# Performance work log

Measured on AMD Instinct MI355X. Metric: run time of the kernel, lower is better.

The kernel has to match this reference:

```python
import jax, jax.numpy as jnp
import numpy as np
import math

B, S, D, V = 16, 512, 64, 32000
MAX_SEQ = 512
TEMP = 1.0
EPS = 1e-12


def setup_inputs() -> dict:
    key = jax.random.key(0)
    k0, k1, k2, k3, k4 = jax.random.split(key, 5)
    tokens = jax.random.randint(k0, (B, S), 0, V)
    token_emb = jax.random.normal(k1, (V, D), dtype=jnp.float32) * 0.02
    lin_w1 = jax.random.normal(k2, (D, D), dtype=jnp.float32) * (1.0 / math.sqrt(D))
    lin_w2 = jax.random.normal(k3, (D, D), dtype=jnp.float32) * (1.0 / math.sqrt(D))
    edge_scale = jnp.full((1,), 0.1, dtype=jnp.float32)  # nn.Parameter init 0.1
    out_w = jax.random.normal(k4, (V, D), dtype=jnp.float32) * 0.02
    return {"tokens": tokens, "token_emb": token_emb, "lin_w1": lin_w1,
            "lin_w2": lin_w2, "edge_scale": edge_scale, "out_w": out_w}


def _embed(tokens, token_emb):
    # polar positional components (seq_len <= max_seq_len branch)
    pos = jnp.arange(S, dtype=jnp.float32)
    thetas = 2.0 * math.pi * (pos / MAX_SEQ)
    rs = 0.3 + 0.6 * (pos / (MAX_SEQ - 1))
    e0 = (rs * jnp.cos(thetas))[None, :, None]          # [1,S,1]
    e1 = (rs * jnp.sin(thetas))[None, :, None]          # [1,S,1]
    tok = token_emb[tokens][:, :, : D - 2]              # [B,S,D-2]
    emb = jnp.concatenate([jnp.broadcast_to(e0, (tok.shape[0], S, 1)),
                           jnp.broadcast_to(e1, (tok.shape[0], S, 1)),
                           tok], axis=-1)               # [B,S,D]
    norms = jnp.sqrt(jnp.clip(jnp.einsum('bsd,bsd->bs', emb, emb), EPS, None))
    return emb / norms[:, :, None]


def _attention(emb):
    # pairwise Euclidean distance attention, diagonal distance zeroed
    n2 = jnp.einsum('bsd,bsd->bs', emb, emb)                      # [B,S]
    dots = jnp.einsum('bqd,bkd->bqk', emb, emb)                   # [B,S,S]
    sq = n2[:, :, None] + n2[:, None, :] - 2.0 * dots
    dist = jnp.sqrt(jnp.clip(sq, EPS, None))
    dist = dist * (1.0 - jnp.eye(S, dtype=dist.dtype))[None]      # eye_mask
    return jax.nn.softmax(-dist / TEMP, axis=-1)                  # [B,S,S]


def reference(tokens, token_emb, lin_w1, lin_w2, edge_scale, out_w):
    emb = _embed(tokens, token_emb)            # [B,S,D]
    attn = _attention(emb)                     # [B,S,S]
    h = emb
    for w in (lin_w1, lin_w2):
        # message passing: x_j -> lin(x_j), edge weight = attn * edge_scale,
        # scatter-add over all incoming edges == batched attn @ h
        h = edge_scale[0] * jnp.einsum('bqk,bkd->bqd', attn, h @ w.T)
    logits = jnp.einsum('bsd,vd->bsv', h, out_w)   # [B,S,V]
    return logits
```

## Files before the change

kernel.cpp:

```cpp
#include <hip/hip_runtime.h>
#include <hip/hip_bf16.h>


#define S_ 512
#define D_ 64
#define V_ 32000

typedef __attribute__((ext_vector_type(8))) __bf16 bf16x8;
typedef __attribute__((ext_vector_type(4))) float f32x4;

__device__ inline unsigned short f2bf(float x) {
    __hip_bfloat16 h = __float2bfloat16(x);
    return __builtin_bit_cast(unsigned short, h);
}

__global__ __launch_bounds__(256) void embed_kernel(const int* __restrict__ tokens,
                                                    const float* __restrict__ temb,
                                                    float* __restrict__ emb,
                                                    float* __restrict__ n2) {
    int row  = blockIdx.x * 4 + (threadIdx.x >> 6);
    int lane = threadIdx.x & 63;
    int s    = row & (S_ - 1);
    int tok  = tokens[row];
    float val;
    if (lane < 2) {
        float fs    = (float)s;
        float theta = 6.283185307179586f * (fs * (1.0f / 512.0f));
        float r     = 0.3f + 0.6f * (fs * (1.0f / 511.0f));
        val = (lane == 0) ? r * cosf(theta) : r * sinf(theta);
    } else {
        val = temb[tok * D_ + lane - 2];
    }
    float ss = val * val;
#pragma unroll
    for (int off = 32; off; off >>= 1) ss += __shfl_xor(ss, off, 64);
    float nrm = sqrtf(fmaxf(ss, 1e-12f));
    float e   = val / nrm;
    emb[row * D_ + lane] = e;
    float nn = e * e;
#pragma unroll
    for (int off = 32; off; off >>= 1) nn += __shfl_xor(nn, off, 64);
    if (lane == 0) n2[row] = nn;
}

__global__ __launch_bounds__(128) void attn_kernel(const float* __restrict__ emb,
                                                   const float* __restrict__ n2,
                                                   float* __restrict__ attn) {
    __shared__ float qs[32][68];
    __shared__ float ks[64][68];
    __shared__ float sc[32][520];
    __shared__ float n2qs[32];
    __shared__ float n2ks[64];
    int b  = blockIdx.x >> 4;
    int q0 = (blockIdx.x & 15) * 32;
    int t  = threadIdx.x;
    const float* ebase = emb + (size_t)b * S_ * D_;
#pragma unroll
    for (int j = 0; j < 4; ++j) {
        int f4 = t + j * 128;
        int r = f4 >> 4, c4 = (f4 & 15) * 4;
        *reinterpret_cast<float4*>(&qs[r][c4]) =
            *reinterpret_cast<const float4*>(&ebase[(q0 + r) * D_ + c4]);
    }
    if (t < 32) n2qs[t] = n2[b * S_ + q0 + t];

    int qg = t >> 4;
    int kg = t & 15;

    for (int kt = 0; kt < 8; ++kt) {
        int k0 = kt * 64;
        __syncthreads();
#pragma unroll
        for (int j = 0; j < 8; ++j) {
            int f4 = t + j * 128;
            int r = f4 >> 4, c4 = (f4 & 15) * 4;
            *reinterpret_cast<float4*>(&ks[r][c4]) =
                *reinterpret_cast<const float4*>(&ebase[(k0 + r) * D_ + c4]);
        }
        if (t < 64) n2ks[t] = n2[b * S_ + k0 + t];
        __syncthreads();

        f32x4 acc[4][4];
#pragma unroll
        for (int i = 0; i < 4; ++i)
#pragma unroll
            for (int j = 0; j < 4; ++j) acc[i][j] = (f32x4){0.f, 0.f, 0.f, 0.f};
#pragma unroll
        for (int dc = 0; dc < 16; ++dc) {
            f32x4 qv[4], kv[4];
#pragma unroll
            for (int i = 0; i < 4; ++i) qv[i] = *reinterpret_cast<f32x4*>(&qs[qg * 4 + i][dc * 4]);
#pragma unroll
            for (int j = 0; j < 4; ++j) kv[j] = *reinterpret_cast<f32x4*>(&ks[kg * 4 + j][dc * 4]);
#pragma unroll
            for (int i = 0; i < 4; ++i)
#pragma unroll
                for (int j = 0; j < 4; ++j) acc[i][j] += qv[i] * kv[j];
        }
#pragma unroll
        for (int i = 0; i < 4; ++i)
#pragma unroll
            for (int j = 0; j < 4; ++j) {
                int q = qg * 4 + i, k = kg * 4 + j;
                f32x4 a = acc[i][j];
                float dot = (a[0] + a[1]) + (a[2] + a[3]);
                float sq  = n2qs[q] + n2ks[k] - 2.0f * dot;
                float sv  = (q0 + q == k0 + k) ? 0.0f : -sqrtf(fmaxf(sq, 1e-12f));
                sc[q][k0 + k] = sv;
            }
    }
    __syncthreads();
    int wave = t >> 6, lane = t & 63;
    for (int r = 0; r < 16; ++r) {
        int q = wave * 16 + r;
        f32x4 ex0, ex1;
        f32x4 v0 = *reinterpret_cast<f32x4*>(&sc[q][lane * 4]);
        f32x4 v1 = *reinterpret_cast<f32x4*>(&sc[q][256 + lane * 4]);
#pragma unroll
        for (int i = 0; i < 4; ++i) { ex0[i] = expf(v0[i]); ex1[i] = expf(v1[i]); }
        float sum = (ex0[0] + ex0[1]) + (ex0[2] + ex0[3]) +
                    (ex1[0] + ex1[1]) + (ex1[2] + ex1[3]);
#pragma unroll
        for (int off = 32; off; off >>= 1) sum += __shfl_xor(sum, off, 64);
        float inv = 1.0f / sum;
        float* row = attn + ((size_t)(b * S_ + q0 + q)) * S_;
        *reinterpret_cast<float4*>(row + lane * 4) =
            make_float4(ex0[0] * inv, ex0[1] * inv, ex0[2] * inv, ex0[3] * inv);
        *reinterpret_cast<float4*>(row + 256 + lane * 4) =
            make_float4(ex1[0] * inv, ex1[1] * inv, ex1[2] * inv, ex1[3] * inv);
    }
}

__global__ __launch_bounds__(256) void proj_kernel(const float* __restrict__ h,
                                                   const float* __restrict__ w,
                                                   float* __restrict__ out) {
    __shared__ float ws[64][68];
    __shared__ float hs[16][68];
    int t  = threadIdx.x;
    int r0 = blockIdx.x * 16;
#pragma unroll
    for (int j = 0; j < 4; ++j) {
        int f4 = t + j * 256;
        int r = f4 >> 4, c4 = (f4 & 15) * 4;
        *reinterpret_cast<float4*>(&ws[r][c4]) =
            *reinterpret_cast<const float4*>(&w[r * D_ + c4]);
    }
    {
        int r = t >> 4, c4 = (t & 15) * 4;
        *reinterpret_cast<float4*>(&hs[r][c4]) =
            *reinterpret_cast<const float4*>(&h[(r0 + r) * D_ + c4]);
    }
    __syncthreads();
    int q = t >> 4, dh = t & 15;
    f32x4 acc[4];
#pragma unroll
    for (int dj = 0; dj < 4; ++dj) acc[dj] = (f32x4){0.f, 0.f, 0.f, 0.f};
#pragma unroll
    for (int ec = 0; ec < 16; ++ec) {
        f32x4 hv = *reinterpret_cast<f32x4*>(&hs[q][ec * 4]);
#pragma unroll
        for (int dj = 0; dj < 4; ++dj) {
            f32x4 wv = *reinterpret_cast<f32x4*>(&ws[dh * 4 + dj][ec * 4]);
            acc[dj] += hv * wv;
        }
    }
    float4 r;
    r.x = (acc[0][0] + acc[0][1]) + (acc[0][2] + acc[0][3]);
    r.y = (acc[1][0] + acc[1][1]) + (acc[1][2] + acc[1][3]);
    r.z = (acc[2][0] + acc[2][1]) + (acc[2][2] + acc[2][3]);
    r.w = (acc[3][0] + acc[3][1]) + (acc[3][2] + acc[3][3]);
    *reinterpret_cast<float4*>(&out[(r0 + q) * D_ + dh * 4]) = r;
}

template <bool BF16OUT>
__global__ __launch_bounds__(128) void prop_kernel(const float* __restrict__ attn,
                                                   const float* __restrict__ tmat,
                                                   const float* __restrict__ edge_scale,
                                                   float* __restrict__ outf,
                                                   unsigned short* __restrict__ outb) {
    __shared__ float As[32][68];
    __shared__ float Ts[64][68];
    int b  = blockIdx.x >> 4;
    int q0 = (blockIdx.x & 15) * 32;
    int t  = threadIdx.x;
    int qg = t >> 4, dh = t & 15;
    f32x4 acc[4];
#pragma unroll
    for (int i = 0; i < 4; ++i) acc[i] = (f32x4){0.f, 0.f, 0.f, 0.f};
    const float* abase = attn + ((size_t)b * S_ + q0) * S_;
    const float* tbase = tmat + (size_t)b * S_ * D_;
    for (int kt = 0; kt < 8; ++kt) {
        int k0 = kt * 64;
        __syncthreads();
#pragma unroll
        for (int j = 0; j < 4; ++j) {
            int f4 = t + j * 128;
            int r = f4 >> 4, c4 = (f4 & 15) * 4;
            *reinterpret_cast<float4*>(&As[r][c4]) =
                *reinterpret_cast<const float4*>(&abase[(size_t)r * S_ + k0 + c4]);
        }
#pragma unroll
        for (int j = 0; j < 8; ++j) {
            int f4 = t + j * 128;
            int r = f4 >> 4, c4 = (f4 & 15) * 4;
            *reinterpret_cast<float4*>(&Ts[r][c4]) =
                *reinterpret_cast<const float4*>(&tbase[(k0 + r) * D_ + c4]);
        }
        __syncthreads();
#pragma unroll
        for (int kc = 0; kc < 16; ++kc) {
            f32x4 tv[4];
#pragma unroll
            for (int ks = 0; ks < 4; ++ks)
                tv[ks] = *reinterpret_cast<f32x4*>(&Ts[kc * 4 + ks][dh * 4]);
#pragma unroll
            for (int i = 0; i < 4; ++i) {
                f32x4 av = *reinterpret_cast<f32x4*>(&As[qg * 4 + i][kc * 4]);
#pragma unroll
                for (int ks = 0; ks < 4; ++ks) acc[i] += av[ks] * tv[ks];
            }
        }
    }
    float scale = edge_scale[0];
#pragma unroll
    for (int i = 0; i < 4; ++i) {
        size_t rowbase = ((size_t)(b * S_ + q0 + qg * 4 + i)) * D_ + dh * 4;
        if (BF16OUT) {
            ushort4 r;
            r.x = f2bf(scale * acc[i][0]); r.y = f2bf(scale * acc[i][1]);
            r.z = f2bf(scale * acc[i][2]); r.w = f2bf(scale * acc[i][3]);
            *reinterpret_cast<ushort4*>(&outb[rowbase]) = r;
        } else {
            *reinterpret_cast<float4*>(&outf[rowbase]) =
                make_float4(scale * acc[i][0], scale * acc[i][1],
                            scale * acc[i][2], scale * acc[i][3]);
        }
    }
}

__global__ __launch_bounds__(256) void cast_kernel(const float* __restrict__ in,
                                                   unsigned short* __restrict__ out, int n) {
    int i = (blockIdx.x * 256 + threadIdx.x) * 4;
    if (i >= n) return;
    float4 v = *reinterpret_cast<const float4*>(in + i);
    ushort4 r;
    r.x = f2bf(v.x); r.y = f2bf(v.y); r.z = f2bf(v.z); r.w = f2bf(v.w);
    *reinterpret_cast<ushort4*>(out + i) = r;
}

__global__ __launch_bounds__(256) void logits_kernel(const unsigned short* __restrict__ hb,
                                                     const unsigned short* __restrict__ wb,
                                                     float* __restrict__ out) {
    __shared__ float Ct[128][132];
    int bid = blockIdx.x;
    int nt = bid % 250, mt = bid / 250;
    int n0 = nt * 128, m0 = mt * 128;
    int wave = threadIdx.x >> 6, lane = threadIdx.x & 63;
    int nw = wave * 32;
    int lr = lane & 15, lh = lane >> 4;

    bf16x8 a[2][2];
#pragma unroll
    for (int ns = 0; ns < 2; ++ns)
#pragma unroll
        for (int kh = 0; kh < 2; ++kh)
            a[ns][kh] = *reinterpret_cast<const bf16x8*>(
                wb + (size_t)(n0 + nw + ns * 16 + lr) * D_ + kh * 32 + lh * 8);

    bf16x8 bfr[8][2];
#pragma unroll
    for (int ms = 0; ms < 8; ++ms)
#pragma unroll
        for (int kh = 0; kh < 2; ++kh)
            bfr[ms][kh] = *reinterpret_cast<const bf16x8*>(
                hb + (size_t)(m0 + ms * 16 + lr) * D_ + kh * 32 + lh * 8);

    f32x4 acc[2][8];
#pragma unroll
    for (int ns = 0; ns < 2; ++ns)
#pragma unroll
        for (int ms = 0; ms < 8; ++ms)
            acc[ns][ms] = (f32x4){0.f, 0.f, 0.f, 0.f};

#pragma unroll
    for (int ns = 0; ns < 2; ++ns)
#pragma unroll
        for (int ms = 0; ms < 8; ++ms) {
            acc[ns][ms] = __builtin_amdgcn_mfma_f32_16x16x32_bf16(a[ns][0], bfr[ms][0], acc[ns][ms], 0, 0, 0);
            acc[ns][ms] = __builtin_amdgcn_mfma_f32_16x16x32_bf16(a[ns][1], bfr[ms][1], acc[ns][ms], 0, 0, 0);
        }

#pragma unroll
    for (int ns = 0; ns < 2; ++ns)
#pragma unroll
        for (int ms = 0; ms < 8; ++ms) {
            f32x4 v = acc[ns][ms];
            *reinterpret_cast<float4*>(&Ct[ms * 16 + lr][nw + ns * 16 + lh * 4]) =
                make_float4(v[0], v[1], v[2], v[3]);
        }
    __syncthreads();

    int t = threadIdx.x;
    int r8 = t >> 5, c = (t & 31) * 4;
#pragma unroll
    for (int j = 0; j < 16; ++j) {
        int row = r8 + j * 8;
        *reinterpret_cast<float4*>(out + (size_t)(m0 + row) * V_ + n0 + c) =
            *reinterpret_cast<float4*>(&Ct[row][c]);
    }
}

extern "C" void kernel_launch(void* const* d_in, const int* in_sizes, int n_in,
                              void* d_out, int out_size, void* d_ws, size_t ws_size,
                              hipStream_t stream) {
    const int*   tokens = (const int*)d_in[0];
    const float* temb   = (const float*)d_in[1];
    const float* w1     = (const float*)d_in[2];
    const float* w2     = (const float*)d_in[3];
    const float* escale = (const float*)d_in[4];
    const float* outw   = (const float*)d_in[5];
    float*       out    = (float*)d_out;

    char* tail = (char*)d_out + 1048576000ull - 23068672ull;
    float* attn = (float*)(tail);
    float* emb  = (float*)(tail + 16777216);
    float* t1   = (float*)(tail + 18874368);
    float* h1   = (float*)(tail + 20971520);

    char* ws = (char*)d_ws;
    unsigned short* hb = (unsigned short*)(ws);
    unsigned short* wb = (unsigned short*)(ws + 1048576);
    float*          n2 = (float*)(ws + 5144576);

    embed_kernel<<<2048, 256, 0, stream>>>(tokens, temb, emb, n2);
    attn_kernel<<<256, 128, 0, stream>>>(emb, n2, attn);
    cast_kernel<<<2000, 256, 0, stream>>>(outw, wb, V_ * D_);
    proj_kernel<<<512, 256, 0, stream>>>(emb, w1, t1);
    prop_kernel<false><<<256, 128, 0, stream>>>(attn, t1, escale, h1, nullptr);
    proj_kernel<<<512, 256, 0, stream>>>(h1, w2, t1);
    prop_kernel<true><<<256, 128, 0, stream>>>(attn, t1, escale, nullptr, hb);
    logits_kernel<<<16000, 256, 0, stream>>>(hb, wb, out);
}
```

Before: 356.4 us.

## Defer softmax normalization into propagation and restructure logits kernel stores

```diff
diff --git a/kernel.cpp b/kernel.cpp
--- a/kernel.cpp
+++ b/kernel.cpp
@@ -45,10 +45,11 @@
 
 __global__ __launch_bounds__(128) void attn_kernel(const float* __restrict__ emb,
                                                    const float* __restrict__ n2,
-                                                   float* __restrict__ attn) {
+                                                   const float* __restrict__ edge_scale,
+                                                   float* __restrict__ attn_u,
+                                                   float* __restrict__ invs) {
     __shared__ float qs[32][68];
     __shared__ float ks[64][68];
-    __shared__ float sc[32][520];
     __shared__ float n2qs[32];
     __shared__ float n2ks[64];
     int b  = blockIdx.x >> 4;
@@ -66,6 +67,7 @@
 
     int qg = t >> 4;
     int kg = t & 15;
+    float rs[4] = {0.f, 0.f, 0.f, 0.f};
 
     for (int kt = 0; kt < 8; ++kt) {
         int k0 = kt * 64;
@@ -98,36 +100,30 @@
                 for (int j = 0; j < 4; ++j) acc[i][j] += qv[i] * kv[j];
         }
 #pragma unroll
-        for (int i = 0; i < 4; ++i)
+        for (int i = 0; i < 4; ++i) {
+            int q = qg * 4 + i;
+            float4 ev;
+            float* evp = &ev.x;
 #pragma unroll
             for (int j = 0; j < 4; ++j) {
-                int q = qg * 4 + i, k = kg * 4 + j;
+                int k = kg * 4 + j;
                 f32x4 a = acc[i][j];
                 float dot = (a[0] + a[1]) + (a[2] + a[3]);
                 float sq  = n2qs[q] + n2ks[k] - 2.0f * dot;
-                float sv  = (q0 + q == k0 + k) ? 0.0f : -sqrtf(fmaxf(sq, 1e-12f));
-                sc[q][k0 + k] = sv;
+                float e   = (q0 + q == k0 + k) ? 1.0f : expf(-sqrtf(fmaxf(sq, 1e-12f)));
+                evp[j] = e;
             }
-    }
-    __syncthreads();
-    int wave = t >> 6, lane = t & 63;
-    for (int r = 0; r < 16; ++r) {
-        int q = wave * 16 + r;
-        f32x4 ex0, ex1;
-        f32x4 v0 = *reinterpret_cast<f32x4*>(&sc[q][lane * 4]);
-        f32x4 v1 = *reinterpret_cast<f32x4*>(&sc[q][256 + lane * 4]);
-#pragma unroll
-        for (int i = 0; i < 4; ++i) { ex0[i] = expf(v0[i]); ex1[i] = expf(v1[i]); }
-        float sum = (ex0[0] + ex0[1]) + (ex0[2] + ex0[3]) +
-                    (ex1[0] + ex1[1]) + (ex1[2] + ex1[3]);
-#pragma unroll
-        for (int off = 32; off; off >>= 1) sum += __shfl_xor(sum, off, 64);
-        float inv = 1.0f / sum;
-        float* row = attn + ((size_t)(b * S_ + q0 + q)) * S_;
-        *reinterpret_cast<float4*>(row + lane * 4) =
-            make_float4(ex0[0] * inv, ex0[1] * inv, ex0[2] * inv, ex0[3] * inv);
-        *reinterpret_cast<float4*>(row + 256 + lane * 4) =
-            make_float4(ex1[0] * inv, ex1[1] * inv, ex1[2] * inv, ex1[3] * inv);
+            rs[i] += (ev.x + ev.y) + (ev.z + ev.w);
+            *reinterpret_cast<float4*>(
+                &attn_u[((size_t)(b * S_ + q0 + q)) * S_ + k0 + kg * 4]) = ev;
+        }
+    }
+    float scale = edge_scale[0];
+#pragma unroll
+    for (int i = 0; i < 4; ++i) {
+#pragma unroll
+        for (int off = 1; off < 16; off <<= 1) rs[i] += __shfl_xor(rs[i], off, 64);
+        if (kg == 0) invs[b * S_ + q0 + qg * 4 + i] = scale / rs[i];
     }
 }
 
@@ -173,9 +169,9 @@
 }
 
 template <bool BF16OUT>
-__global__ __launch_bounds__(128) void prop_kernel(const float* __restrict__ attn,
+__global__ __launch_bounds__(128) void prop_kernel(const float* __restrict__ attn_u,
                                                    const float* __restrict__ tmat,
-                                                   const float* __restrict__ edge_scale,
+                                                   const float* __restrict__ invs,
                                                    float* __restrict__ outf,
                                                    unsigned short* __restrict__ outb) {
     __shared__ float As[32][68];
@@ -187,7 +183,7 @@
     f32x4 acc[4];
 #pragma unroll
     for (int i = 0; i < 4; ++i) acc[i] = (f32x4){0.f, 0.f, 0.f, 0.f};
-    const float* abase = attn + ((size_t)b * S_ + q0) * S_;
+    const float* abase = attn_u + ((size_t)b * S_ + q0) * S_;
     const float* tbase = tmat + (size_t)b * S_ * D_;
     for (int kt = 0; kt < 8; ++kt) {
         int k0 = kt * 64;
@@ -221,19 +217,20 @@
             }
         }
     }
-    float scale = edge_scale[0];
 #pragma unroll
     for (int i = 0; i < 4; ++i) {
-        size_t rowbase = ((size_t)(b * S_ + q0 + qg * 4 + i)) * D_ + dh * 4;
+        int row = b * S_ + q0 + qg * 4 + i;
+        float inv = invs[row];
+        size_t rowbase = (size_t)row * D_ + dh * 4;
         if (BF16OUT) {
             ushort4 r;
-            r.x = f2bf(scale * acc[i][0]); r.y = f2bf(scale * acc[i][1]);
-            r.z = f2bf(scale * acc[i][2]); r.w = f2bf(scale * acc[i][3]);
+            r.x = f2bf(inv * acc[i][0]); r.y = f2bf(inv * acc[i][1]);
+            r.z = f2bf(inv * acc[i][2]); r.w = f2bf(inv * acc[i][3]);
             *reinterpret_cast<ushort4*>(&outb[rowbase]) = r;
         } else {
             *reinterpret_cast<float4*>(&outf[rowbase]) =
-                make_float4(scale * acc[i][0], scale * acc[i][1],
-                            scale * acc[i][2], scale * acc[i][3]);
+                make_float4(inv * acc[i][0], inv * acc[i][1],
+                            inv * acc[i][2], inv * acc[i][3]);
         }
     }
 }
@@ -251,12 +248,12 @@
 __global__ __launch_bounds__(256) void logits_kernel(const unsigned short* __restrict__ hb,
                                                      const unsigned short* __restrict__ wb,
                                                      float* __restrict__ out) {
-    __shared__ float Ct[128][132];
-    int bid = blockIdx.x;
-    int nt = bid % 250, mt = bid / 250;
-    int n0 = nt * 128, m0 = mt * 128;
+    int orig = blockIdx.x;
+    int wg   = (orig & 7) * 1000 + (orig >> 3);
+    int nt = wg % 250, mt = wg / 250;
+    int n0 = nt * 128, m0 = mt * 256;
     int wave = threadIdx.x >> 6, lane = threadIdx.x & 63;
-    int nw = wave * 32;
+    int nw = n0 + wave * 32;
     int lr = lane & 15, lh = lane >> 4;
 
     bf16x8 a[2][2];
@@ -265,48 +262,22 @@
 #pragma unroll
         for (int kh = 0; kh < 2; ++kh)
             a[ns][kh] = *reinterpret_cast<const bf16x8*>(
-                wb + (size_t)(n0 + nw + ns * 16 + lr) * D_ + kh * 32 + lh * 8);
-
-    bf16x8 bfr[8][2];
-#pragma unroll
-    for (int ms = 0; ms < 8; ++ms)
-#pragma unroll
-        for (int kh = 0; kh < 2; ++kh)
-            bfr[ms][kh] = *reinterpret_cast<const bf16x8*>(
-                hb + (size_t)(m0 + ms * 16 + lr) * D_ + kh * 32 + lh * 8);
-
-    f32x4 acc[2][8];
-#pragma unroll
-    for (int ns = 0; ns < 2; ++ns)
-#pragma unroll
-        for (int ms = 0; ms < 8; ++ms)
-            acc[ns][ms] = (f32x4){0.f, 0.f, 0.f, 0.f};
-
-#pragma unroll
-    for (int ns = 0; ns < 2; ++ns)
-#pragma unroll
-        for (int ms = 0; ms < 8; ++ms) {
-            acc[ns][ms] = __builtin_amdgcn_mfma_f32_16x16x32_bf16(a[ns][0], bfr[ms][0], acc[ns][ms], 0, 0, 0);
-            acc[ns][ms] = __builtin_amdgcn_mfma_f32_16x16x32_bf16(a[ns][1], bfr[ms][1], acc[ns][ms], 0, 0, 0);
-        }
-
-#pragma unroll
-    for (int ns = 0; ns < 2; ++ns)
-#pragma unroll
-        for (int ms = 0; ms < 8; ++ms) {
-            f32x4 v = acc[ns][ms];
-            *reinterpret_cast<float4*>(&Ct[ms * 16 + lr][nw + ns * 16 + lh * 4]) =
-                make_float4(v[0], v[1], v[2], v[3]);
-        }
-    __syncthreads();
-
-    int t = threadIdx.x;
-    int r8 = t >> 5, c = (t & 31) * 4;
-#pragma unroll
-    for (int j = 0; j < 16; ++j) {
-        int row = r8 + j * 8;
-        *reinterpret_cast<float4*>(out + (size_t)(m0 + row) * V_ + n0 + c) =
-            *reinterpret_cast<float4*>(&Ct[row][c]);
+                wb + (size_t)(nw + ns * 16 + lr) * D_ + kh * 32 + lh * 8);
+
+#pragma unroll 4
+    for (int ms = 0; ms < 16; ++ms) {
+        const unsigned short* hrow = hb + (size_t)(m0 + ms * 16 + lr) * D_ + lh * 8;
+        bf16x8 b0 = *reinterpret_cast<const bf16x8*>(hrow);
+        bf16x8 b1 = *reinterpret_cast<const bf16x8*>(hrow + 32);
+        f32x4 acc0 = (f32x4){0.f, 0.f, 0.f, 0.f};
+        f32x4 acc1 = (f32x4){0.f, 0.f, 0.f, 0.f};
+        acc0 = __builtin_amdgcn_mfma_f32_16x16x32_bf16(a[0][0], b0, acc0, 0, 0, 0);
+        acc0 = __builtin_amdgcn_mfma_f32_16x16x32_bf16(a[0][1], b1, acc0, 0, 0, 0);
+        acc1 = __builtin_amdgcn_mfma_f32_16x16x32_bf16(a[1][0], b0, acc1, 0, 0, 0);
+        acc1 = __builtin_amdgcn_mfma_f32_16x16x32_bf16(a[1][1], b1, acc1, 0, 0, 0);
+        size_t rowoff = (size_t)(m0 + ms * 16 + lr) * V_;
+        __builtin_nontemporal_store(acc0, reinterpret_cast<f32x4*>(out + rowoff + nw + lh * 4));
+        __builtin_nontemporal_store(acc1, reinterpret_cast<f32x4*>(out + rowoff + nw + 16 + lh * 4));
     }
 }
 
@@ -328,16 +299,17 @@
     float* h1   = (float*)(tail + 20971520);
 
     char* ws = (char*)d_ws;
-    unsigned short* hb = (unsigned short*)(ws);
-    unsigned short* wb = (unsigned short*)(ws + 1048576);
-    float*          n2 = (float*)(ws + 5144576);
+    unsigned short* hb   = (unsigned short*)(ws);
+    unsigned short* wb   = (unsigned short*)(ws + 1048576);
+    float*          n2   = (float*)(ws + 5144576);
+    float*          invs = (float*)(ws + 5177344);
 
     embed_kernel<<<2048, 256, 0, stream>>>(tokens, temb, emb, n2);
-    attn_kernel<<<256, 128, 0, stream>>>(emb, n2, attn);
+    attn_kernel<<<256, 128, 0, stream>>>(emb, n2, escale, attn, invs);
     cast_kernel<<<2000, 256, 0, stream>>>(outw, wb, V_ * D_);
     proj_kernel<<<512, 256, 0, stream>>>(emb, w1, t1);
-    prop_kernel<false><<<256, 128, 0, stream>>>(attn, t1, escale, h1, nullptr);
+    prop_kernel<false><<<256, 128, 0, stream>>>(attn, t1, invs, h1, nullptr);
     proj_kernel<<<512, 256, 0, stream>>>(h1, w2, t1);
-    prop_kernel<true><<<256, 128, 0, stream>>>(attn, t1, escale, nullptr, hb);
-    logits_kernel<<<16000, 256, 0, stream>>>(hb, wb, out);
-}
+    prop_kernel<true><<<256, 128, 0, stream>>>(attn, t1, invs, nullptr, hb);
+    logits_kernel<<<8000, 256, 0, stream>>>(hb, wb, out);
+}
```

Result: slower. 491.4 us (+37.9%).
